# Performance work log

Measured on AMD Instinct MI355X. Metric: run time of the kernel, lower is better.

The kernel has to match this reference:

```python
import jax, jax.numpy as jnp
import numpy as np

EPS = 1e-5  # torch LayerNorm default eps

def _mish(x):
    return x * jnp.tanh(jax.nn.softplus(x))

def _ln(x, g, b):
    mu = jnp.mean(x, axis=-1, keepdims=True)
    var = jnp.mean(jnp.square(x - mu), axis=-1, keepdims=True)
    return (x - mu) * jax.lax.rsqrt(var + EPS) * g + b

def setup_inputs() -> dict:
    key = jax.random.key(0)
    ks = jax.random.split(key, 10)
    B, D, O1, O2, O3 = 65536, 784, 512, 264, 128
    def lin(k, fan_in, shape):
        bound = 1.0 / np.sqrt(fan_in)
        return jax.random.uniform(k, shape, jnp.float32, -bound, bound)
    return {
        "x":  jax.random.uniform(ks[0], (B, D), jnp.float32),
        "W1": lin(ks[1], D,  (O1, D)),   # enFC1, bias=False
        "g1": jnp.ones((O1,), jnp.float32), "b1": jnp.zeros((O1,), jnp.float32),
        "W2": lin(ks[2], O1, (O2, O1)),  # enFC2, bias=False
        "g2": jnp.ones((O2,), jnp.float32), "b2": jnp.zeros((O2,), jnp.float32),
        "W3": lin(ks[3], O2, (O3, O2)),  # enFC3 with bias
        "b3": lin(ks[4], O2, (O3,)),
        "gh": jnp.ones((O3,), jnp.float32), "bh": jnp.zeros((O3,), jnp.float32),
        "D1": lin(ks[5], O3, (O2, O3)),  # deFC1, bias=False
        "g3": jnp.ones((O2,), jnp.float32), "b3n": jnp.zeros((O2,), jnp.float32),
        "D2": lin(ks[6], O2, (O1, O2)),  # deFC2, bias=False
        "g4": jnp.ones((O1,), jnp.float32), "b4": jnp.zeros((O1,), jnp.float32),
        "D3": lin(ks[7], O1, (D, O1)),   # deFC3 with bias
        "bo": lin(ks[8], O1, (D,)),
    }

def reference(x, W1, g1, b1, W2, g2, b2, W3, b3, gh, bh,
              D1, g3, b3n, D2, g4, b4, D3, bo):
    h = _mish(_ln(x @ W1.T, g1, b1))
    h = _mish(_ln(h @ W2.T, g2, b2))
    x_latent = _mish(_ln(h @ W3.T + b3, gh, bh))
    h = _mish(_ln(x_latent @ D1.T, g3, b3n))
    h = _mish(_ln(h @ D2.T, g4, b4))
    out = jax.nn.sigmoid(h @ D3.T + bo)
    return out, jnp.sum(jnp.abs(x_latent))
```

## Files before the change

kernel.cpp:

```cpp
#include <hip/hip_runtime.h>


typedef short bf16x8 __attribute__((ext_vector_type(8)));
typedef float f32x4  __attribute__((ext_vector_type(4)));

#define B_ROWS 65536
#define EPS_LN 1e-5f

static __device__ __forceinline__ unsigned short f2bf(float f) {
    union { float f; unsigned u; } v; v.f = f;
    unsigned r = v.u + 0x7FFFu + ((v.u >> 16) & 1u);
    return (unsigned short)(r >> 16);
}

static __device__ __forceinline__ float mish_f(float x) {
    if (x > 15.f) return x;
    float u = __expf(x);
    float p = __fmaf_rn(u, u, 2.f * u);
    return x * (p / (p + 2.f));
}

static __device__ __forceinline__ void glds16(const void* g, void* l) {
    typedef __attribute__((address_space(3))) unsigned lds_u32;
    typedef __attribute__((address_space(1))) const unsigned glb_u32;
    lds_u32* lp = (lds_u32*)l;
    unsigned lofs = __builtin_amdgcn_readfirstlane((unsigned)(unsigned long long)lp);
    lp = (lds_u32*)(unsigned long long)lofs;
    __builtin_amdgcn_global_load_lds((glb_u32*)g, lp, 16, 0, 0);
}

struct CvtArgs {
    const float* src[6];
    unsigned short* dst[6];
    int O[6], K[6], KP[6];
    int base[7];
};

__global__ void wpad_kernel(CvtArgs a) {
    int b = blockIdx.x;
    int seg = 0;
    while (b >= a.base[seg + 1]) ++seg;
    int r = b - a.base[seg];
    int O = a.O[seg], K = a.K[seg], KP = a.KP[seg];
    const float* s = a.src[seg];
    unsigned short* d = a.dst[seg];
    for (int c = threadIdx.x; c < KP; c += 256) {
        unsigned short v = 0;
        if (r < O && c < K) v = f2bf(s[(size_t)r * K + c]);
        d[(size_t)r * KP + c] = v;
    }
}

template<int KP, int ASTR, int BN, int OREAL, int OSTRIDE, int NKT,
         bool SRCF32, bool HASBIAS, bool ABS, bool LN>
__global__ __launch_bounds__(512, 2)
void layer9(const void* __restrict__ Asrc,
            const unsigned short* __restrict__ Wp,
            const float* __restrict__ gam,
            const float* __restrict__ bet,
            const float* __restrict__ bias,
            void* __restrict__ Aout,
            float* __restrict__ partials)
{
    constexpr int NT   = BN / 64;
    constexpr int NCHW = BN / 8;
    constexpr int NCH  = NCHW + (SRCF32 ? 0 : 16);
    constexpr int MAXC = (NCH + 7) / 8;
    constexpr int ABY  = 128 * 128;
    constexpr int WBY  = BN * 128;

    __shared__ __align__(16) char smem[2 * ABY + 2 * WBY];

    const int tid  = threadIdx.x;
    const int lane = tid & 63;
    const int wu   = __builtin_amdgcn_readfirstlane(tid >> 6);
    const int wr = wu >> 2, wc = wu & 3;
    const int lg = lane >> 4, lc = lane & 15;
    const int row0  = blockIdx.x * 128;
    const int cbase = LN ? 0 : blockIdx.y * BN;

    const int crow = lane >> 3;
    const int sg   = (lane & 7) ^ crow;
    const size_t vofW = ((size_t)crow * KP + (size_t)(sg << 3)) * 2;
    const size_t vofA = ((size_t)crow * ASTR + (size_t)(sg << 3)) * 2;

    auto stage = [&](int t, int b) {
#pragma unroll
        for (int i = 0; i < MAXC; ++i) {
            int c = wu + 8 * i;
            if (c < NCHW) {
                const char* g = (const char*)Wp +
                    ((size_t)(cbase + c * 8) * KP) * 2 + (size_t)t * 128 + vofW;
                glds16(g, smem + (2 * ABY + b * WBY + c * 1024));
            } else if (c < NCH) {
                int ca = c - NCHW;
                const char* g = (const char*)Asrc +
                    ((size_t)(row0 + ca * 8) * ASTR) * 2 + (size_t)t * 128 + vofA;
                glds16(g, smem + (b * ABY + ca * 1024));
            }
        }
    };

    const int ar = tid >> 2, as = tid & 3;
    const float* axp = (const float*)Asrc + (size_t)(row0 + ar) * ASTR + as * 16;
    float4 rA[4];
#pragma unroll
    for (int j = 0; j < 4; ++j) rA[j] = make_float4(0, 0, 0, 0);

    auto loadA1 = [&](int t) {
#pragma unroll
        for (int j = 0; j < 4; ++j) {
            int c0 = t * 64 + as * 16 + j * 4;
            rA[j] = (c0 + 3 < 784) ? *(const float4*)(axp + t * 64 + j * 4)
                                   : make_float4(0, 0, 0, 0);
        }
    };
    auto pubA = [&](int b) {
        union { unsigned short us[8]; uint4 v; } u0, u1;
        u0.us[0] = f2bf(rA[0].x); u0.us[1] = f2bf(rA[0].y);
        u0.us[2] = f2bf(rA[0].z); u0.us[3] = f2bf(rA[0].w);
        u0.us[4] = f2bf(rA[1].x); u0.us[5] = f2bf(rA[1].y);
        u0.us[6] = f2bf(rA[1].z); u0.us[7] = f2bf(rA[1].w);
        u1.us[0] = f2bf(rA[2].x); u1.us[1] = f2bf(rA[2].y);
        u1.us[2] = f2bf(rA[2].z); u1.us[3] = f2bf(rA[2].w);
        u1.us[4] = f2bf(rA[3].x); u1.us[5] = f2bf(rA[3].y);
        u1.us[6] = f2bf(rA[3].z); u1.us[7] = f2bf(rA[3].w);
        int s0 = as * 2, rb = b * ABY + ar * 128, rx = ar & 7;
        *(uint4*)(smem + rb + (((s0    ) ^ rx) << 4)) = u0.v;
        *(uint4*)(smem + rb + (((s0 + 1) ^ rx) << 4)) = u1.v;
    };

    stage(0, 0);
    if constexpr (SRCF32) { loadA1(0); pubA(0); }
    __syncthreads();

    f32x4 acc[4][NT];
#pragma unroll
    for (int a = 0; a < 4; ++a)
#pragma unroll
        for (int c = 0; c < NT; ++c) acc[a][c] = (f32x4){0.f, 0.f, 0.f, 0.f};

    const int f0 = ((lg ^ (lc & 7)) << 4);

    for (int t = 0; t < NKT; ++t) {
        const int bsel = t & 1;
        if (t + 1 < NKT) {
            stage(t + 1, bsel ^ 1);
            if constexpr (SRCF32) loadA1(t + 1);
        }
        const char* Ab = smem + bsel * ABY + (wr * 64 + lc) * 128;
        const char* Bb = smem + 2 * ABY + bsel * WBY + (wc * NT * 16 + lc) * 128;
#pragma unroll
        for (int h = 0; h < 2; ++h) {
            const int fh = f0 ^ (h << 6);
            bf16x8 afr[4], bfr[NT];
#pragma unroll
            for (int a = 0; a < 4; ++a)
                afr[a] = *(const bf16x8*)(Ab + a * 2048 + fh);
#pragma unroll
            for (int c = 0; c < NT; ++c)
                bfr[c] = *(const bf16x8*)(Bb + c * 2048 + fh);
            __builtin_amdgcn_s_setprio(1);
#pragma unroll
            for (int c = 0; c < NT; ++c)
#pragma unroll
                for (int a = 0; a < 4; ++a)
                    acc[a][c] = __builtin_amdgcn_mfma_f32_16x16x32_bf16(afr[a], bfr[c], acc[a][c], 0, 0, 0);
            __builtin_amdgcn_s_setprio(0);
        }
        if constexpr (SRCF32) { if (t + 1 < NKT) pubA(bsel ^ 1); }
        __syncthreads();
    }

    if constexpr (LN) {
        if constexpr (HASBIAS) {
#pragma unroll
            for (int c = 0; c < NT; ++c) {
                int col = wc * NT * 16 + c * 16 + lc;
                float bv = (col < OREAL) ? bias[col] : 0.f;
#pragma unroll
                for (int a = 0; a < 4; ++a)
#pragma unroll
                    for (int r = 0; r < 4; ++r) acc[a][c][r] += bv;
            }
        }
        float ps1[4][4], ps2[4][4];
#pragma unroll
        for (int a = 0; a < 4; ++a)
#pragma unroll
            for (int r = 0; r < 4; ++r) { ps1[a][r] = 0.f; ps2[a][r] = 0.f; }
#pragma unroll
        for (int a = 0; a < 4; ++a)
#pragma unroll
            for (int c = 0; c < NT; ++c)
#pragma unroll
                for (int r = 0; r < 4; ++r) {
                    float v = acc[a][c][r];
                    ps1[a][r] += v;
                    ps2[a][r] = __fmaf_rn(v, v, ps2[a][r]);
                }
#pragma unroll
        for (int m = 1; m < 16; m <<= 1)
#pragma unroll
            for (int a = 0; a < 4; ++a)
#pragma unroll
                for (int r = 0; r < 4; ++r) {
                    ps1[a][r] += __shfl_xor(ps1[a][r], m);
                    ps2[a][r] += __shfl_xor(ps2[a][r], m);
                }

        float* lnP  = (float*)smem;
        float* lnMR = (float*)(smem + 4096);
        float* wsum = (float*)(smem + 5120);

        if (lc == 0) {
#pragma unroll
            for (int a = 0; a < 4; ++a)
#pragma unroll
                for (int r = 0; r < 4; ++r) {
                    int row = wr * 64 + a * 16 + lg * 4 + r;
                    lnP[row * 4 + wc]       = ps1[a][r];
                    lnP[512 + row * 4 + wc] = ps2[a][r];
                }
        }
        __syncthreads();
        if (tid < 128) {
            float s1 = lnP[tid * 4] + lnP[tid * 4 + 1] + lnP[tid * 4 + 2] + lnP[tid * 4 + 3];
            float s2 = lnP[512 + tid * 4] + lnP[512 + tid * 4 + 1] +
                       lnP[512 + tid * 4 + 2] + lnP[512 + tid * 4 + 3];
            float mu = s1 * (1.f / OREAL);
            float var = fmaxf(s2 * (1.f / OREAL) - mu * mu, 0.f);
            lnMR[tid]       = mu;
            lnMR[128 + tid] = rsqrtf(var + EPS_LN);
        }
        __syncthreads();

        float gcol[NT], bcol[NT];
#pragma unroll
        for (int c = 0; c < NT; ++c) {
            int col = wc * NT * 16 + c * 16 + lc;
            gcol[c] = (col < OREAL) ? gam[col] : 0.f;
            bcol[c] = (col < OREAL) ? bet[col] : 0.f;
        }

        float asum = 0.f;
        unsigned short* outp = (unsigned short*)Aout;
#pragma unroll
        for (int a = 0; a < 4; ++a)
#pragma unroll
            for (int r = 0; r < 4; ++r) {
                int rl = wr * 64 + a * 16 + lg * 4 + r;
                float mu = lnMR[rl], rs = lnMR[128 + rl];
                size_t rowoff = (size_t)(row0 + rl) * OSTRIDE;
#pragma unroll
                for (int c = 0; c < NT; ++c) {
                    int col = wc * NT * 16 + c * 16 + lc;
                    if (col < OSTRIDE) {
                        unsigned short outv = 0;
                        if (col < OREAL) {
                            float v = (acc[a][c][r] - mu) * rs * gcol[c] + bcol[c];
                            float mz = mish_f(v);
                            if (ABS) asum += fabsf(mz);
                            outv = f2bf(mz);
                        }
                        outp[rowoff + col] = outv;
                    }
                }
            }

        if constexpr (ABS) {
#pragma unroll
            for (int m = 1; m < 64; m <<= 1) asum += __shfl_xor(asum, m);
            if (lane == 0) wsum[wu] = asum;
            __syncthreads();
            if (tid == 0) {
                float s = 0.f;
                for (int w = 0; w < 8; ++w) s += wsum[w];
                partials[blockIdx.x] = s;
            }
        }
    } else {
        float* outp = (float*)Aout;
#pragma unroll
        for (int c = 0; c < NT; ++c) {
            int col = cbase + wc * NT * 16 + c * 16 + lc;
            bool ok = col < OREAL;
            float bv = ok ? bias[col] : 0.f;
#pragma unroll
            for (int a = 0; a < 4; ++a)
#pragma unroll
                for (int r = 0; r < 4; ++r) {
                    if (ok) {
                        int rl = wr * 64 + a * 16 + lg * 4 + r;
                        float v = acc[a][c][r] + bv;
                        outp[(size_t)(row0 + rl) * OSTRIDE + col] = 1.f / (1.f + __expf(-v));
                    }
                }
        }
    }
}

__global__ void reduce_abs(const float* __restrict__ partials, float* __restrict__ out) {
    __shared__ float sm[256];
    float s = 0.f;
    for (int i = threadIdx.x; i < 512; i += 256) s += partials[i];
    sm[threadIdx.x] = s;
    __syncthreads();
    for (int step = 128; step > 0; step >>= 1) {
        if (threadIdx.x < step) sm[threadIdx.x] += sm[threadIdx.x + step];
        __syncthreads();
    }
    if (threadIdx.x == 0) out[0] = sm[0];
}

extern "C" void kernel_launch(void* const* d_in, const int* in_sizes, int n_in,
                              void* d_out, int out_size, void* d_ws, size_t ws_size,
                              hipStream_t stream)
{
    const float* x   = (const float*)d_in[0];
    const float* W1  = (const float*)d_in[1];
    const float* g1  = (const float*)d_in[2];
    const float* b1  = (const float*)d_in[3];
    const float* W2  = (const float*)d_in[4];
    const float* g2  = (const float*)d_in[5];
    const float* b2  = (const float*)d_in[6];
    const float* W3  = (const float*)d_in[7];
    const float* b3  = (const float*)d_in[8];
    const float* gh  = (const float*)d_in[9];
    const float* bh  = (const float*)d_in[10];
    const float* D1  = (const float*)d_in[11];
    const float* g3  = (const float*)d_in[12];
    const float* b3n = (const float*)d_in[13];
    const float* D2  = (const float*)d_in[14];
    const float* g4  = (const float*)d_in[15];
    const float* b4  = (const float*)d_in[16];
    const float* D3  = (const float*)d_in[17];
    const float* bo  = (const float*)d_in[18];

    char* ws = (char*)d_ws;
    size_t off = 0;
    auto alloc = [&](size_t bytes) -> char* {
        char* p = ws + off;
        off += (bytes + 255) & ~(size_t)255;
        return p;
    };
    unsigned short* W1p = (unsigned short*)alloc((size_t)512 * 832 * 2);
    unsigned short* W2p = (unsigned short*)alloc((size_t)384 * 512 * 2);
    unsigned short* W3p = (unsigned short*)alloc((size_t)128 * 320 * 2);
    unsigned short* D1p = (unsigned short*)alloc((size_t)384 * 128 * 2);
    unsigned short* D2p = (unsigned short*)alloc((size_t)512 * 320 * 2);
    unsigned short* D3p = (unsigned short*)alloc((size_t)896 * 512 * 2);
    unsigned short* actP = (unsigned short*)alloc((size_t)B_ROWS * 512 * 2);
    unsigned short* actQ = (unsigned short*)alloc((size_t)B_ROWS * 320 * 2);
    unsigned short* actL = (unsigned short*)alloc((size_t)B_ROWS * 128 * 2);
    float* partials = (float*)alloc(512 * 4);

    CvtArgs ca;
    ca.src[0] = W1; ca.dst[0] = W1p; ca.O[0] = 512; ca.K[0] = 784; ca.KP[0] = 832;
    ca.src[1] = W2; ca.dst[1] = W2p; ca.O[1] = 264; ca.K[1] = 512; ca.KP[1] = 512;
    ca.src[2] = W3; ca.dst[2] = W3p; ca.O[2] = 128; ca.K[2] = 264; ca.KP[2] = 320;
    ca.src[3] = D1; ca.dst[3] = D1p; ca.O[3] = 264; ca.K[3] = 128; ca.KP[3] = 128;
    ca.src[4] = D2; ca.dst[4] = D2p; ca.O[4] = 512; ca.K[4] = 264; ca.KP[4] = 320;
    ca.src[5] = D3; ca.dst[5] = D3p; ca.O[5] = 784; ca.K[5] = 512; ca.KP[5] = 512;
    ca.base[0] = 0;    ca.base[1] = 512;  ca.base[2] = 896;
    ca.base[3] = 1024; ca.base[4] = 1408; ca.base[5] = 1920; ca.base[6] = 2816;
    wpad_kernel<<<2816, 256, 0, stream>>>(ca);

    const int NB = B_ROWS / 128;

    layer9<832, 784, 512, 512, 512, 13, true,  false, false, true>
        <<<NB, 512, 0, stream>>>(x, W1p, g1, b1, nullptr, actP, nullptr);
    layer9<512, 512, 384, 264, 320, 8,  false, false, false, true>
        <<<NB, 512, 0, stream>>>(actP, W2p, g2, b2, nullptr, actQ, nullptr);
    layer9<320, 320, 128, 128, 128, 5,  false, true,  true,  true>
        <<<NB, 512, 0, stream>>>(actQ, W3p, gh, bh, b3, actL, partials);
    layer9<128, 128, 384, 264, 320, 2,  false, false, false, true>
        <<<NB, 512, 0, stream>>>(actL, D1p, g3, b3n, nullptr, actQ, nullptr);
    layer9<320, 320, 512, 512, 512, 5,  false, false, false, true>
        <<<NB, 512, 0, stream>>>(actQ, D2p, g4, b4, nullptr, actP, nullptr);
    dim3 g6(NB, 2);
    layer9<512, 512, 448, 784, 784, 8,  false, true,  false, false>
        <<<g6, 512, 0, stream>>>(actP, D3p, nullptr, nullptr, bo, d_out, nullptr);

    reduce_abs<<<1, 256, 0, stream>>>(partials, (float*)d_out + (size_t)B_ROWS * 784);
}
```

Before: 426.9 us.

## Fuse layers 2-4 into one kernel keeping intermediates in shared memory

Replaces the three separate layer kernels for enFC2, enFC3 and deFC1 with one 'trio' kernel. Each 128-row block keeps the 264-wide and latent activations in LDS instead of round-tripping them through global memory. The enFC3 K padding shrinks from 320 to 288 to cut wasted MFMA work. This removes two launches and about 100 MB of global traffic. In exchange it uses a large LDS footprint (136 KB per block), which may limit occupancy.

```diff
diff --git a/kernel.cpp b/kernel.cpp
--- a/kernel.cpp
+++ b/kernel.cpp
@@ -297,6 +297,358 @@
                     }
                 }
         }
+    }
+}
+
+__global__ __launch_bounds__(512, 2)
+void trio(const unsigned short* __restrict__ actP,
+          const unsigned short* __restrict__ W2p,
+          const unsigned short* __restrict__ W3p,
+          const unsigned short* __restrict__ D1p,
+          const float* __restrict__ g2, const float* __restrict__ b2,
+          const float* __restrict__ gh, const float* __restrict__ bh,
+          const float* __restrict__ b3,
+          const float* __restrict__ g3, const float* __restrict__ b3n,
+          unsigned short* __restrict__ actQ,
+          float* __restrict__ partials)
+{
+    __shared__ __align__(16) char smem[139264];
+
+    const int tid  = threadIdx.x;
+    const int lane = tid & 63;
+    const int wu   = __builtin_amdgcn_readfirstlane(tid >> 6);
+    const int wr = wu >> 2, wc = wu & 3;
+    const int lg = lane >> 4, lc = lane & 15;
+    const int row0 = blockIdx.x * 128;
+
+    const int sgl = (lane & 3) ^ ((lane >> 3) & 3);
+    const size_t vofA  = ((size_t)(lane >> 2) * 512 + (size_t)(sgl << 3)) * 2;
+    const size_t vofW2 = vofA;
+    const size_t vofW3 = ((size_t)(lane >> 2) * 288 + (size_t)(sgl << 3)) * 2;
+    const size_t vofD1 = ((size_t)(lane >> 2) * 128 + (size_t)(sgl << 3)) * 2;
+
+    const int fswz = ((lg ^ ((lc >> 1) & 3)) << 4);
+
+    float* lnP  = (float*)smem;
+    float* lnMR = (float*)(smem + 4096);
+    float* wsum = (float*)(smem + 5120);
+
+    auto ln_stats = [&](float ps1[4][4], float ps2[4][4], float invO) {
+#pragma unroll
+        for (int m = 1; m < 16; m <<= 1)
+#pragma unroll
+            for (int a = 0; a < 4; ++a)
+#pragma unroll
+                for (int r = 0; r < 4; ++r) {
+                    ps1[a][r] += __shfl_xor(ps1[a][r], m);
+                    ps2[a][r] += __shfl_xor(ps2[a][r], m);
+                }
+        if (lc == 0) {
+#pragma unroll
+            for (int a = 0; a < 4; ++a)
+#pragma unroll
+                for (int r = 0; r < 4; ++r) {
+                    int row = wr * 64 + a * 16 + lg * 4 + r;
+                    lnP[row * 4 + wc]       = ps1[a][r];
+                    lnP[512 + row * 4 + wc] = ps2[a][r];
+                }
+        }
+        __syncthreads();
+        if (tid < 128) {
+            float s1 = lnP[tid * 4] + lnP[tid * 4 + 1] + lnP[tid * 4 + 2] + lnP[tid * 4 + 3];
+            float s2 = lnP[512 + tid * 4] + lnP[512 + tid * 4 + 1] +
+                       lnP[512 + tid * 4 + 2] + lnP[512 + tid * 4 + 3];
+            float mu = s1 * invO;
+            float var = fmaxf(s2 * invO - mu * mu, 0.f);
+            lnMR[tid]       = mu;
+            lnMR[128 + tid] = rsqrtf(var + EPS_LN);
+        }
+        __syncthreads();
+    };
+
+    {
+        constexpr int NT = 6;
+        f32x4 acc[4][NT];
+#pragma unroll
+        for (int a = 0; a < 4; ++a)
+#pragma unroll
+            for (int c = 0; c < NT; ++c) acc[a][c] = (f32x4){0.f, 0.f, 0.f, 0.f};
+
+        auto stage1 = [&](int t, int b) {
+#pragma unroll
+            for (int i = 0; i < 4; ++i) {
+                int c = wu + 8 * i;
+                if (c < 24) {
+                    const char* g = (const char*)W2p +
+                        ((size_t)(c * 16) * 512) * 2 + (size_t)t * 64 + vofW2;
+                    glds16(g, smem + (16384 + b * 24576 + c * 1024));
+                } else {
+                    int ca = c - 24;
+                    const char* g = (const char*)actP +
+                        ((size_t)(row0 + ca * 16) * 512) * 2 + (size_t)t * 64 + vofA;
+                    glds16(g, smem + (b * 8192 + ca * 1024));
+                }
+            }
+        };
+
+        stage1(0, 0);
+        __syncthreads();
+        for (int t = 0; t < 16; ++t) {
+            const int bsel = t & 1;
+            if (t + 1 < 16) stage1(t + 1, bsel ^ 1);
+            const char* Ab = smem + bsel * 8192 + (wr * 64 + lc) * 64 + fswz;
+            const char* Bb = smem + 16384 + bsel * 24576 + (wc * 96 + lc) * 64 + fswz;
+            bf16x8 afr[4], bfr[NT];
+#pragma unroll
+            for (int a = 0; a < 4; ++a) afr[a] = *(const bf16x8*)(Ab + a * 1024);
+#pragma unroll
+            for (int c = 0; c < NT; ++c) bfr[c] = *(const bf16x8*)(Bb + c * 1024);
+            __builtin_amdgcn_s_setprio(1);
+#pragma unroll
+            for (int c = 0; c < NT; ++c)
+#pragma unroll
+                for (int a = 0; a < 4; ++a)
+                    acc[a][c] = __builtin_amdgcn_mfma_f32_16x16x32_bf16(afr[a], bfr[c], acc[a][c], 0, 0, 0);
+            __builtin_amdgcn_s_setprio(0);
+            __syncthreads();
+        }
+
+        float ps1[4][4], ps2[4][4];
+#pragma unroll
+        for (int a = 0; a < 4; ++a)
+#pragma unroll
+            for (int r = 0; r < 4; ++r) { ps1[a][r] = 0.f; ps2[a][r] = 0.f; }
+#pragma unroll
+        for (int a = 0; a < 4; ++a)
+#pragma unroll
+            for (int c = 0; c < NT; ++c)
+#pragma unroll
+                for (int r = 0; r < 4; ++r) {
+                    float v = acc[a][c][r];
+                    ps1[a][r] += v;
+                    ps2[a][r] = __fmaf_rn(v, v, ps2[a][r]);
+                }
+        ln_stats(ps1, ps2, 1.f / 264);
+
+        float gcol[NT], bcol[NT];
+#pragma unroll
+        for (int c = 0; c < NT; ++c) {
+            int col = wc * 96 + c * 16 + lc;
+            gcol[c] = (col < 264) ? g2[col] : 0.f;
+            bcol[c] = (col < 264) ? b2[col] : 0.f;
+        }
+#pragma unroll
+        for (int a = 0; a < 4; ++a)
+#pragma unroll
+            for (int r = 0; r < 4; ++r) {
+                int rl = wr * 64 + a * 16 + lg * 4 + r;
+                float mu = lnMR[rl], rs = lnMR[128 + rl];
+                int sx = (rl >> 1) & 3;
+                int rowb = 65536 + rl * 576;
+#pragma unroll
+                for (int c = 0; c < NT; ++c) {
+                    int col = wc * 96 + c * 16 + lc;
+                    if (col < 288) {
+                        unsigned short outv = 0;
+                        if (col < 264) {
+                            float v = (acc[a][c][r] - mu) * rs * gcol[c] + bcol[c];
+                            outv = f2bf(mish_f(v));
+                        }
+                        int byte = rowb + ((col >> 5) << 6) +
+                                   ((((col >> 3) & 3) ^ sx) << 4) + ((col & 7) << 1);
+                        *(unsigned short*)(smem + byte) = outv;
+                    }
+                }
+            }
+        __syncthreads();
+    }
+
+    {
+        constexpr int NT = 2;
+        f32x4 acc[4][NT];
+#pragma unroll
+        for (int a = 0; a < 4; ++a)
+#pragma unroll
+            for (int c = 0; c < NT; ++c) acc[a][c] = (f32x4){0.f, 0.f, 0.f, 0.f};
+
+        auto stage2 = [&](int t, int b) {
+            int c = wu;
+            const char* g = (const char*)W3p +
+                ((size_t)(c * 16) * 288) * 2 + (size_t)t * 64 + vofW3;
+            glds16(g, smem + (b * 8192 + c * 1024));
+        };
+
+        stage2(0, 0);
+        __syncthreads();
+        for (int t = 0; t < 9; ++t) {
+            const int bsel = t & 1;
+            if (t + 1 < 9) stage2(t + 1, bsel ^ 1);
+            const char* Ab = smem + 65536 + (wr * 64 + lc) * 576 + t * 64 + fswz;
+            const char* Bb = smem + bsel * 8192 + (wc * 32 + lc) * 64 + fswz;
+            bf16x8 afr[4], bfr[NT];
+#pragma unroll
+            for (int a = 0; a < 4; ++a) afr[a] = *(const bf16x8*)(Ab + a * 16 * 576);
+#pragma unroll
+            for (int c = 0; c < NT; ++c) bfr[c] = *(const bf16x8*)(Bb + c * 1024);
+            __builtin_amdgcn_s_setprio(1);
+#pragma unroll
+            for (int c = 0; c < NT; ++c)
+#pragma unroll
+                for (int a = 0; a < 4; ++a)
+                    acc[a][c] = __builtin_amdgcn_mfma_f32_16x16x32_bf16(afr[a], bfr[c], acc[a][c], 0, 0, 0);
+            __builtin_amdgcn_s_setprio(0);
+            __syncthreads();
+        }
+
+#pragma unroll
+        for (int c = 0; c < NT; ++c) {
+            int col = wc * 32 + c * 16 + lc;
+            float bv = b3[col];
+#pragma unroll
+            for (int a = 0; a < 4; ++a)
+#pragma unroll
+                for (int r = 0; r < 4; ++r) acc[a][c][r] += bv;
+        }
+        float ps1[4][4], ps2[4][4];
+#pragma unroll
+        for (int a = 0; a < 4; ++a)
+#pragma unroll
+            for (int r = 0; r < 4; ++r) { ps1[a][r] = 0.f; ps2[a][r] = 0.f; }
+#pragma unroll
+        for (int a = 0; a < 4; ++a)
+#pragma unroll
+            for (int c = 0; c < NT; ++c)
+#pragma unroll
+                for (int r = 0; r < 4; ++r) {
+                    float v = acc[a][c][r];
+                    ps1[a][r] += v;
+                    ps2[a][r] = __fmaf_rn(v, v, ps2[a][r]);
+                }
+        ln_stats(ps1, ps2, 1.f / 128);
+
+        float gcol[NT], bcol[NT];
+#pragma unroll
+        for (int c = 0; c < NT; ++c) {
+            int col = wc * 32 + c * 16 + lc;
+            gcol[c] = gh[col];
+            bcol[c] = bh[col];
+        }
+        float asum = 0.f;
+#pragma unroll
+        for (int a = 0; a < 4; ++a)
+#pragma unroll
+            for (int r = 0; r < 4; ++r) {
+                int rl = wr * 64 + a * 16 + lg * 4 + r;
+                float mu = lnMR[rl], rs = lnMR[128 + rl];
+                int sx = (rl >> 1) & 3;
+                int rowb = 16384 + rl * 256;
+#pragma unroll
+                for (int c = 0; c < NT; ++c) {
+                    int col = wc * 32 + c * 16 + lc;
+                    float v = (acc[a][c][r] - mu) * rs * gcol[c] + bcol[c];
+                    float mz = mish_f(v);
+                    asum += fabsf(mz);
+                    int byte = rowb + ((col >> 5) << 6) +
+                               ((((col >> 3) & 3) ^ sx) << 4) + ((col & 7) << 1);
+                    *(unsigned short*)(smem + byte) = f2bf(mz);
+                }
+            }
+#pragma unroll
+        for (int m = 1; m < 64; m <<= 1) asum += __shfl_xor(asum, m);
+        if (lane == 0) wsum[wu] = asum;
+        __syncthreads();
+        if (tid == 0) {
+            float s = 0.f;
+            for (int w = 0; w < 8; ++w) s += wsum[w];
+            partials[blockIdx.x] = s;
+        }
+        __syncthreads();
+    }
+
+    {
+        constexpr int NT = 6;
+        f32x4 acc[4][NT];
+#pragma unroll
+        for (int a = 0; a < 4; ++a)
+#pragma unroll
+            for (int c = 0; c < NT; ++c) acc[a][c] = (f32x4){0.f, 0.f, 0.f, 0.f};
+
+        auto stage3 = [&](int t, int b) {
+#pragma unroll
+            for (int i = 0; i < 3; ++i) {
+                int c = wu + 8 * i;
+                const char* g = (const char*)D1p +
+                    ((size_t)(c * 16) * 128) * 2 + (size_t)t * 64 + vofD1;
+                glds16(g, smem + (65536 + b * 24576 + c * 1024));
+            }
+        };
+
+        stage3(0, 0);
+        __syncthreads();
+        for (int t = 0; t < 4; ++t) {
+            const int bsel = t & 1;
+            if (t + 1 < 4) stage3(t + 1, bsel ^ 1);
+            const char* Ab = smem + 16384 + (wr * 64 + lc) * 256 + t * 64 + fswz;
+            const char* Bb = smem + 65536 + bsel * 24576 + (wc * 96 + lc) * 64 + fswz;
+            bf16x8 afr[4], bfr[NT];
+#pragma unroll
+            for (int a = 0; a < 4; ++a) afr[a] = *(const bf16x8*)(Ab + a * 16 * 256);
+#pragma unroll
+            for (int c = 0; c < NT; ++c) bfr[c] = *(const bf16x8*)(Bb + c * 1024);
+            __builtin_amdgcn_s_setprio(1);
+#pragma unroll
+            for (int c = 0; c < NT; ++c)
+#pragma unroll
+                for (int a = 0; a < 4; ++a)
+                    acc[a][c] = __builtin_amdgcn_mfma_f32_16x16x32_bf16(afr[a], bfr[c], acc[a][c], 0, 0, 0);
+            __builtin_amdgcn_s_setprio(0);
+            __syncthreads();
+        }
+
+        float ps1[4][4], ps2[4][4];
+#pragma unroll
+        for (int a = 0; a < 4; ++a)
+#pragma unroll
+            for (int r = 0; r < 4; ++r) { ps1[a][r] = 0.f; ps2[a][r] = 0.f; }
+#pragma unroll
+        for (int a = 0; a < 4; ++a)
+#pragma unroll
+            for (int c = 0; c < NT; ++c)
+#pragma unroll
+                for (int r = 0; r < 4; ++r) {
+                    float v = acc[a][c][r];
+                    ps1[a][r] += v;
+                    ps2[a][r] = __fmaf_rn(v, v, ps2[a][r]);
+                }
+        ln_stats(ps1, ps2, 1.f / 264);
+
+        float gcol[NT], bcol[NT];
+#pragma unroll
+        for (int c = 0; c < NT; ++c) {
+            int col = wc * 96 + c * 16 + lc;
+            gcol[c] = (col < 264) ? g3[col] : 0.f;
+            bcol[c] = (col < 264) ? b3n[col] : 0.f;
+        }
+#pragma unroll
+        for (int a = 0; a < 4; ++a)
+#pragma unroll
+            for (int r = 0; r < 4; ++r) {
+                int rl = wr * 64 + a * 16 + lg * 4 + r;
+                float mu = lnMR[rl], rs = lnMR[128 + rl];
+                size_t rowoff = (size_t)(row0 + rl) * 320;
+#pragma unroll
+                for (int c = 0; c < NT; ++c) {
+                    int col = wc * 96 + c * 16 + lc;
+                    if (col < 320) {
+                        unsigned short outv = 0;
+                        if (col < 264) {
+                            float v = (acc[a][c][r] - mu) * rs * gcol[c] + bcol[c];
+                            outv = f2bf(mish_f(v));
+                        }
+                        actQ[rowoff + col] = outv;
+                    }
+                }
+            }
     }
 }
 
@@ -346,19 +698,18 @@
     };
     unsigned short* W1p = (unsigned short*)alloc((size_t)512 * 832 * 2);
     unsigned short* W2p = (unsigned short*)alloc((size_t)384 * 512 * 2);
-    unsigned short* W3p = (unsigned short*)alloc((size_t)128 * 320 * 2);
+    unsigned short* W3p = (unsigned short*)alloc((size_t)128 * 288 * 2);
     unsigned short* D1p = (unsigned short*)alloc((size_t)384 * 128 * 2);
     unsigned short* D2p = (unsigned short*)alloc((size_t)512 * 320 * 2);
     unsigned short* D3p = (unsigned short*)alloc((size_t)896 * 512 * 2);
     unsigned short* actP = (unsigned short*)alloc((size_t)B_ROWS * 512 * 2);
     unsigned short* actQ = (unsigned short*)alloc((size_t)B_ROWS * 320 * 2);
-    unsigned short* actL = (unsigned short*)alloc((size_t)B_ROWS * 128 * 2);
     float* partials = (float*)alloc(512 * 4);
 
     CvtArgs ca;
     ca.src[0] = W1; ca.dst[0] = W1p; ca.O[0] = 512; ca.K[0] = 784; ca.KP[0] = 832;
     ca.src[1] = W2; ca.dst[1] = W2p; ca.O[1] = 264; ca.K[1] = 512; ca.KP[1] = 512;
-    ca.src[2] = W3; ca.dst[2] = W3p; ca.O[2] = 128; ca.K[2] = 264; ca.KP[2] = 320;
+    ca.src[2] = W3; ca.dst[2] = W3p; ca.O[2] = 128; ca.K[2] = 264; ca.KP[2] = 288;
     ca.src[3] = D1; ca.dst[3] = D1p; ca.O[3] = 264; ca.K[3] = 128; ca.KP[3] = 128;
     ca.src[4] = D2; ca.dst[4] = D2p; ca.O[4] = 512; ca.K[4] = 264; ca.KP[4] = 320;
     ca.src[5] = D3; ca.dst[5] = D3p; ca.O[5] = 784; ca.K[5] = 512; ca.KP[5] = 512;
@@ -370,12 +721,8 @@
 
     layer9<832, 784, 512, 512, 512, 13, true,  false, false, true>
         <<<NB, 512, 0, stream>>>(x, W1p, g1, b1, nullptr, actP, nullptr);
-    layer9<512, 512, 384, 264, 320, 8,  false, false, false, true>
-        <<<NB, 512, 0, stream>>>(actP, W2p, g2, b2, nullptr, actQ, nullptr);
-    layer9<320, 320, 128, 128, 128, 5,  false, true,  true,  true>
-        <<<NB, 512, 0, stream>>>(actQ, W3p, gh, bh, b3, actL, partials);
-    layer9<128, 128, 384, 264, 320, 2,  false, false, false, true>
-        <<<NB, 512, 0, stream>>>(actL, D1p, g3, b3n, nullptr, actQ, nullptr);
+    trio<<<NB, 512, 0, stream>>>(actP, W2p, W3p, D1p,
+                                 g2, b2, gh, bh, b3, g3, b3n, actQ, partials);
     layer9<320, 320, 512, 512, 512, 5,  false, false, false, true>
         <<<NB, 512, 0, stream>>>(actQ, D2p, g4, b4, nullptr, actP, nullptr);
     dim3 g6(NB, 2);
```

After: 421.8 us. About the same (-1.2%).
